# Performance work log

Hardware: AMD Instinct MI355X
Metric: run time of the kernel (lower is better)

The kernel has to match this reference:

```python
import jax, jax.numpy as jnp
import numpy as np
from jax.ops import segment_sum

N_NODES = 50000
N_EDGES = 50000
N_GRAPHS = 1024


def _inv_deg(idx, num_segments):
    deg = segment_sum(jnp.ones(idx.shape[0], jnp.float32), idx, num_segments=num_segments)
    return jnp.where(deg > 0, 1.0 / deg, 0.0)


def hypergraph_conv(x, W, b, node_idx, edge_idx):
    # PyG HypergraphConv (use_attention=False, heads=1, hyperedge_weight=1):
    # out = D^{-1} H B^{-1} H^T (X W) + b
    D = _inv_deg(node_idx, N_NODES)   # inverse node degree [N]
    B = _inv_deg(edge_idx, N_EDGES)   # inverse hyperedge degree [E]
    xl = x @ W                         # [N, out]
    # node -> hyperedge aggregation
    edge_feat = B[:, None] * segment_sum(xl[node_idx], edge_idx, num_segments=N_EDGES)
    # hyperedge -> node aggregation
    out = D[:, None] * segment_sum(edge_feat[edge_idx], node_idx, num_segments=N_NODES)
    return out + b


def global_mean_pool(x, batch):
    s = segment_sum(x, batch, num_segments=N_GRAPHS)
    cnt = segment_sum(jnp.ones(x.shape[0], jnp.float32), batch, num_segments=N_GRAPHS)
    return s / jnp.maximum(cnt, 1.0)[:, None]


def setup_inputs() -> dict:
    key = jax.random.key(0)
    ks = jax.random.split(key, 16)
    F, H = 128, 256
    def lin(k, fi, fo):
        s = 1.0 / np.sqrt(fi)
        k1, k2 = jax.random.split(k)
        return (jax.random.uniform(k1, (fi, fo), jnp.float32, -s, s),
                jax.random.uniform(k2, (fo,), jnp.float32, -s, s))
    W1, b1 = lin(ks[0], F, H)
    W2, b2 = lin(ks[1], H, 2 * H)
    W3, b3 = lin(ks[2], 2 * H, H)
    Wl1, bl1 = lin(ks[3], H, H // 2)
    Wl2, bl2 = lin(ks[4], H // 2, 1)
    x = jax.random.normal(ks[5], (N_NODES, F), jnp.float32)
    hyperedge_index = jax.random.randint(ks[6], (2, 400000), 0, N_EDGES, jnp.int64)
    batch = jnp.sort(jax.random.randint(ks[7], (N_NODES,), 0, N_GRAPHS, jnp.int64))
    return {"x": x, "hyperedge_index": hyperedge_index, "batch": batch,
            "W1": W1, "b1": b1, "W2": W2, "b2": b2, "W3": W3, "b3": b3,
            "Wl1": Wl1, "bl1": bl1, "Wl2": Wl2, "bl2": bl2}


def reference(x, hyperedge_index, batch, W1, b1, W2, b2, W3, b3, Wl1, bl1, Wl2, bl2):
    node_idx, edge_idx = hyperedge_index[0], hyperedge_index[1]
    h = jax.nn.relu(hypergraph_conv(x, W1, b1, node_idx, edge_idx))
    h = jax.nn.relu(hypergraph_conv(h, W2, b2, node_idx, edge_idx))
    h = jax.nn.relu(hypergraph_conv(h, W3, b3, node_idx, edge_idx))
    g = global_mean_pool(h, batch)              # [G, H]
    g = jax.nn.relu(g @ Wl1 + bl1)
    out = g @ Wl2 + bl2                          # [G, 1]
    return out
```

## Files before the change

### kernel.cpp

```cpp
#include <hip/hip_runtime.h>
#include <hip/hip_bf16.h>

#define N_NODES  50000
#define N_EDGES  50000
#define N_INC    400000
#define N_GRAPHS 1024
#define M_PAD    50048
#define SEG_CAP  50176

typedef __bf16 bf16x8 __attribute__((ext_vector_type(8)));
typedef float  f32x4  __attribute__((ext_vector_type(4)));

__device__ __forceinline__ unsigned short f2bf(float f) {
    __hip_bfloat16 h = __float2bfloat16(f);
    return __builtin_bit_cast(unsigned short, h);
}
__device__ __forceinline__ float bflo(unsigned int u) {
    return __builtin_bit_cast(float, u << 16);
}
__device__ __forceinline__ float bfhi(unsigned int u) {
    return __builtin_bit_cast(float, u & 0xffff0000u);
}
__device__ __forceinline__ unsigned int packbf(float a, float b) {
    return (unsigned int)f2bf(a) | ((unsigned int)f2bf(b) << 16);
}
__device__ __forceinline__ void load_lds16(const unsigned short* g, unsigned short* l) {
    __builtin_amdgcn_global_load_lds((const __attribute__((address_space(1))) void*)g,
                                     (__attribute__((address_space(3))) void*)l, 16, 0, 0);
}

#define NB_INC  1563
#define NB_CONV 6250
#define NB_W1   128
#define NB_W2   512
#define NB_W3   512
__global__ __launch_bounds__(256) void normhist_kernel(const int* __restrict__ hei,
                                                       int* __restrict__ nidx, int* __restrict__ eidx,
                                                       unsigned short* __restrict__ rn,
                                                       unsigned short* __restrict__ re,
                                                       int* __restrict__ ndeg_p, int* __restrict__ edeg_p,
                                                       const float* __restrict__ x,
                                                       unsigned short* __restrict__ xbf,
                                                       const float* __restrict__ W1, unsigned short* __restrict__ wt1,
                                                       const float* __restrict__ W2, unsigned short* __restrict__ wt2,
                                                       const float* __restrict__ W3, unsigned short* __restrict__ wt3) {
    int b = blockIdx.x, t = threadIdx.x;
    if (b < NB_INC) {
        __shared__ int s32;
        if (t == 0) s32 = 0;
        __syncthreads();
        int probe = hei[4 * t + 1] | hei[4 * t + 3];
        if (probe) s32 = 1;
        __syncthreads();
        int is32 = s32;
        int i = b * 256 + t;
        if (i < N_INC) {
            int n, e;
            if (is32) { n = hei[i];     e = hei[N_INC + i]; }
            else      { n = hei[2 * i]; e = hei[2 * N_INC + 2 * i]; }
            nidx[i] = n; eidx[i] = e;
            rn[i] = (unsigned short)atomicAdd(&ndeg_p[n << 4], 1);
            re[i] = (unsigned short)atomicAdd(&edeg_p[e << 4], 1);
        }
    } else if (b < NB_INC + NB_CONV) {
        int i = (b - NB_INC) * 256 + t;
        float4 v = *(const float4*)(x + 4 * (size_t)i);
        ushort4 o;
        o.x = f2bf(v.x); o.y = f2bf(v.y); o.z = f2bf(v.z); o.w = f2bf(v.w);
        *(ushort4*)(xbf + 4 * (size_t)i) = o;
    } else if (b < NB_INC + NB_CONV + NB_W1) {
        int i = (b - NB_INC - NB_CONV) * 256 + t;
        int k = i >> 8, n = i & 255;
        wt1[n * 128 + k] = f2bf(W1[i]);
    } else if (b < NB_INC + NB_CONV + NB_W1 + NB_W2) {
        int i = (b - NB_INC - NB_CONV - NB_W1) * 256 + t;
        int k = i >> 9, n = i & 511;
        wt2[n * 256 + k] = f2bf(W2[i]);
    } else {
        int i = (b - NB_INC - NB_CONV - NB_W1 - NB_W2) * 256 + t;
        int k = i >> 8, n = i & 255;
        wt3[n * 512 + k] = f2bf(W3[i]);
    }
}

__global__ __launch_bounds__(256) void scan_up_f(const int* __restrict__ edeg_p,
                                                 const int* __restrict__ ndeg_p,
                                                 const int* __restrict__ hei,
                                                 const int* __restrict__ braw,
                                                 int* __restrict__ eoff, int* __restrict__ noff,
                                                 int* __restrict__ goff,
                                                 int* __restrict__ partials) {
    int b = blockIdx.x, t = threadIdx.x;
    if (b >= 98) {
        __shared__ int s32;
        if (t == 0) s32 = 0;
        __syncthreads();
        int probe = hei[4 * t + 1] | hei[4 * t + 3];
        if (probe) s32 = 1;
        __syncthreads();
        int is32 = s32;
        int g = (b - 98) * 256 + t;
        int lo = 0, hi = N_NODES;
        while (lo < hi) {
            int mid = (lo + hi) >> 1;
            int v = is32 ? braw[mid] : braw[2 * mid];
            if (v < g) lo = mid + 1; else hi = mid;
        }
        goff[g] = lo;
        if (g == 1023) goff[1024] = N_NODES;
        return;
    }
    __shared__ int lds[256];
    const int* in; int* outp; int lb;
    if (b < 49) { in = edeg_p; outp = eoff; lb = b; }
    else        { in = ndeg_p; outp = noff; lb = b - 49; }
    int base = lb * 1024 + t * 4;
    int4 v;
    v.x = in[(size_t)(base + 0) << 4];
    v.y = in[(size_t)(base + 1) << 4];
    v.z = in[(size_t)(base + 2) << 4];
    v.w = in[(size_t)(base + 3) << 4];
    int s = v.x + v.y + v.z + v.w;
    lds[t] = s;
    __syncthreads();
    for (int off = 1; off < 256; off <<= 1) {
        int u = (t >= off) ? lds[t - off] : 0;
        __syncthreads();
        lds[t] += u;
        __syncthreads();
    }
    int excl = lds[t] - s;
    if (t == 255) partials[b] = lds[255];
    int4 o;
    o.x = excl;
    o.y = excl + v.x;
    o.z = o.y + v.y;
    o.w = o.z + v.z;
    *(int4*)(outp + base) = o;
}

__global__ __launch_bounds__(128) void scan_mid_f(int* __restrict__ partials) {
    __shared__ int lds[98];
    int t = threadIdx.x;
    if (t < 98) lds[t] = partials[t];
    __syncthreads();
    if (t < 2) {
        int lo = t * 49, hi = lo + 49;
        int run = 0;
        for (int i = lo; i < hi; ++i) { int x = lds[i]; lds[i] = run; run += x; }
    }
    __syncthreads();
    if (t < 98) partials[t] = lds[t];
}

__global__ __launch_bounds__(256) void scan_down_f(int* __restrict__ eoff,
                                                   int* __restrict__ noff,
                                                   const int* __restrict__ partials) {
    int b = blockIdx.x, t = threadIdx.x;
    int* outp; int lb;
    if (b < 49) { outp = eoff; lb = b; }
    else        { outp = noff; lb = b - 49; }
    int base = lb * 1024 + t * 4;
    int p = partials[b];
    int4 v = *(const int4*)(outp + base);
    v.x += p; v.y += p; v.z += p; v.w += p;
    *(int4*)(outp + base) = v;
}

__global__ __launch_bounds__(256) void prep_kernel(const int* __restrict__ nidx,
                                                   const int* __restrict__ eidx,
                                                   const unsigned short* __restrict__ rn,
                                                   const unsigned short* __restrict__ re,
                                                   const int* __restrict__ eoff,
                                                   const int* __restrict__ noff,
                                                   unsigned short* __restrict__ csre,
                                                   unsigned short* __restrict__ csrn) {
    int i = blockIdx.x * 256 + threadIdx.x;
    if (i >= N_INC) return;
    int n = nidx[i], e = eidx[i];
    csre[eoff[e] + re[i]] = (unsigned short)n;
    csrn[noff[n] + rn[i]] = (unsigned short)e;
}

template <bool EPI>
__global__ __launch_bounds__(256) void gemm128_kernel(const unsigned short* __restrict__ A,
                                                      const unsigned short* __restrict__ Bt,
                                                      const float* __restrict__ bias,
                                                      unsigned short* __restrict__ C,
                                                      int M, int K, int N) {
    __shared__ unsigned short As[128 * 32];
    __shared__ unsigned short Bs[128 * 32];
    __shared__ unsigned short Cs[32][140];
    int tid  = threadIdx.x;
    int wave = tid >> 6, lane = tid & 63;
    int n0 = blockIdx.x * 128, m0 = blockIdx.y * 128;
    int quad = lane >> 4, fr = lane & 15;
    int wr = wave >> 1, wc = wave & 1;
    int lrow16 = lane >> 2;
    int lchunk = (lane & 3) * 8;

    const unsigned short* gsrc;
    unsigned short* ldst;
    if (wave < 2) { gsrc = A  + (size_t)(m0 + wave * 64) * K;       ldst = As + wave * 64 * 32; }
    else          { gsrc = Bt + (size_t)(n0 + (wave - 2) * 64) * K; ldst = Bs + (wave - 2) * 64 * 32; }

    f32x4 acc[4][4];
#pragma unroll
    for (int s = 0; s < 4; ++s)
#pragma unroll
        for (int c = 0; c < 4; ++c) acc[s][c] = (f32x4){0.f, 0.f, 0.f, 0.f};

    for (int k0 = 0; k0 < K; k0 += 32) {
#pragma unroll
        for (int l = 0; l < 4; ++l) {
            const unsigned short* g = gsrc + (size_t)(l * 16 + lrow16) * K + k0 + lchunk;
            load_lds16(g, ldst + l * 16 * 32);
        }
        __syncthreads();
        bf16x8 af[4], bfr[4];
#pragma unroll
        for (int s = 0; s < 4; ++s)
            af[s] = *(const bf16x8*)&As[(wr * 64 + s * 16 + fr) * 32 + quad * 8];
#pragma unroll
        for (int c = 0; c < 4; ++c)
            bfr[c] = *(const bf16x8*)&Bs[(wc * 64 + c * 16 + fr) * 32 + quad * 8];
#pragma unroll
        for (int s = 0; s < 4; ++s)
#pragma unroll
            for (int c = 0; c < 4; ++c)
                acc[s][c] = __builtin_amdgcn_mfma_f32_16x16x32_bf16(af[s], bfr[c], acc[s][c], 0, 0, 0);
        __syncthreads();
    }

    float bv[4];
#pragma unroll
    for (int c = 0; c < 4; ++c) bv[c] = EPI ? bias[n0 + wc * 64 + c * 16 + fr] : 0.f;
#pragma unroll
    for (int s = 0; s < 4; ++s) {
#pragma unroll
        for (int c = 0; c < 4; ++c)
#pragma unroll
            for (int r = 0; r < 4; ++r) {
                float v = acc[s][c][r];
                if (EPI) v = fmaxf(v + bv[c], 0.f);
                Cs[wr * 16 + quad * 4 + r][wc * 64 + c * 16 + fr] = f2bf(v);
            }
        __syncthreads();
#pragma unroll
        for (int i = 0; i < 2; ++i) {
            int rl  = i * 16 + (tid >> 4);
            int col = (tid & 15) * 8;
            int gm  = m0 + (rl >> 4) * 64 + s * 16 + (rl & 15);
            if (gm < M) {
                uint4 v = *(const uint4*)&Cs[rl][col];
                *(uint4*)&C[(size_t)gm * N + n0 + col] = v;
            }
        }
        __syncthreads();
    }
}

template <int C, bool BIAS>
__device__ __forceinline__ void seg_body(const unsigned short* __restrict__ in,
                                         const int* __restrict__ offs,
                                         const int* __restrict__ degs_p,
                                         const unsigned short* __restrict__ csr_src,
                                         const float* __restrict__ bias,
                                         unsigned short* __restrict__ outp,
                                         int nseg) {
    constexpr int VEC = C / 64;
    constexpr int NW  = VEC / 2;
    int w = (blockIdx.x * 256 + threadIdx.x) >> 6;
    int lane = threadIdx.x & 63;
    if (w >= nseg) return;
    int deg   = __builtin_amdgcn_readfirstlane(degs_p[(size_t)w << 4]);
    int start = __builtin_amdgcn_readfirstlane(offs[w]);
    float dinv = (deg > 0) ? 1.0f / (float)deg : 0.0f;
    const unsigned short* cs = csr_src + start;
    float acc[VEC];
#pragma unroll
    for (int q = 0; q < VEC; ++q) acc[q] = 0.f;
    size_t lbase = (size_t)lane * VEC;

    auto accum = [&](unsigned int* v) {
#pragma unroll
        for (int q = 0; q < NW; ++q) { acc[2 * q] += bflo(v[q]); acc[2 * q + 1] += bfhi(v[q]); }
    };
    auto loadrow = [&](int src, unsigned int* v) {
        const unsigned int* p = (const unsigned int*)(in + (size_t)src * C + lbase);
        if constexpr (NW == 4)      { uint4 t = *(const uint4*)p; v[0] = t.x; v[1] = t.y; v[2] = t.z; v[3] = t.w; }
        else if constexpr (NW == 2) { uint2 t = *(const uint2*)p; v[0] = t.x; v[1] = t.y; }
        else                        { v[0] = *p; }
    };

    int j = 0;
    for (; j + 8 <= deg; j += 8) {
        int s[8];
        unsigned int v[8][NW];
#pragma unroll
        for (int u = 0; u < 8; ++u) s[u] = __builtin_amdgcn_readfirstlane((int)cs[j + u]);
#pragma unroll
        for (int u = 0; u < 8; ++u) loadrow(s[u], v[u]);
        __asm__ __volatile__("" ::: "memory");
#pragma unroll
        for (int u = 0; u < 8; ++u) accum(v[u]);
    }
    for (; j + 4 <= deg; j += 4) {
        int s[4];
        unsigned int v[4][NW];
#pragma unroll
        for (int u = 0; u < 4; ++u) s[u] = __builtin_amdgcn_readfirstlane((int)cs[j + u]);
#pragma unroll
        for (int u = 0; u < 4; ++u) loadrow(s[u], v[u]);
        __asm__ __volatile__("" ::: "memory");
#pragma unroll
        for (int u = 0; u < 4; ++u) accum(v[u]);
    }
    for (; j < deg; ++j) {
        int s0 = __builtin_amdgcn_readfirstlane((int)cs[j]);
        unsigned int v0[NW];
        loadrow(s0, v0);
        accum(v0);
    }

    unsigned int o[NW];
#pragma unroll
    for (int q = 0; q < NW; ++q) {
        float a = acc[2 * q] * dinv;
        float b = acc[2 * q + 1] * dinv;
        if constexpr (BIAS) {
            a = fmaxf(a + bias[lbase + 2 * q], 0.f);
            b = fmaxf(b + bias[lbase + 2 * q + 1], 0.f);
        }
        o[q] = packbf(a, b);
    }
    unsigned int* po = (unsigned int*)(outp + (size_t)w * C + lbase);
    if constexpr (NW == 4)      { *(uint4*)po = make_uint4(o[0], o[1], o[2], o[3]); }
    else if constexpr (NW == 2) { *(uint2*)po = make_uint2(o[0], o[1]); }
    else                        { *po = o[0]; }
}

template <int C>
__global__ __launch_bounds__(256) void seg_edge_t(const unsigned short* __restrict__ xl,
                                                  const int* __restrict__ eoff,
                                                  const int* __restrict__ edeg_p,
                                                  const unsigned short* __restrict__ csr_src,
                                                  unsigned short* __restrict__ ef) {
    seg_body<C, false>(xl, eoff, edeg_p, csr_src, nullptr, ef, N_EDGES);
}

template <int C, bool BIAS>
__global__ __launch_bounds__(256) void seg_node_t(const unsigned short* __restrict__ ef,
                                                  const int* __restrict__ noff,
                                                  const int* __restrict__ ndeg_p,
                                                  const unsigned short* __restrict__ csr_src,
                                                  const float* __restrict__ bias,
                                                  unsigned short* __restrict__ hout) {
    seg_body<C, BIAS>(ef, noff, ndeg_p, csr_src, bias, hout, N_NODES);
}

__global__ __launch_bounds__(256) void pool_head_kernel(const unsigned short* __restrict__ h,
                                                        const int* __restrict__ goff,
                                                        const float* __restrict__ Wl1,
                                                        const float* __restrict__ bl1,
                                                        const float* __restrict__ Wl2,
                                                        const float* __restrict__ bl2,
                                                        float* __restrict__ out) {
    __shared__ float xs[256];
    __shared__ float red[128];
    int g = blockIdx.x, t = threadIdx.x;
    int s = goff[g], cnt = goff[g + 1] - s;
    float acc = 0.f;
    for (int i = 0; i < cnt; ++i) {
        unsigned int u = h[(size_t)(s + i) * 256 + t];
        acc += __builtin_bit_cast(float, u << 16);
    }
    xs[t] = acc / (float)(cnt > 0 ? cnt : 1);
    __syncthreads();
    if (t < 128) {
        float s2 = 0.f;
        for (int f = 0; f < 256; ++f) s2 += xs[f] * Wl1[f * 128 + t];
        s2 = fmaxf(s2 + bl1[t], 0.f);
        red[t] = s2 * Wl2[t];
    }
    __syncthreads();
    for (int off = 64; off > 0; off >>= 1) {
        if (t < off) red[t] += red[t + off];
        __syncthreads();
    }
    if (t == 0) out[g] = red[0] + bl2[0];
}

extern "C" void kernel_launch(void* const* d_in, const int* in_sizes, int n_in,
                              void* d_out, int out_size, void* d_ws, size_t ws_size,
                              hipStream_t stream) {
    const float* x     = (const float*)d_in[0];
    const int* hei     = (const int*)d_in[1];
    const int* braw    = (const int*)d_in[2];
    const float* W1    = (const float*)d_in[3];
    const float* b1    = (const float*)d_in[4];
    const float* W2    = (const float*)d_in[5];
    const float* b2    = (const float*)d_in[6];
    const float* W3    = (const float*)d_in[7];
    const float* b3    = (const float*)d_in[8];
    const float* Wl1   = (const float*)d_in[9];
    const float* bl1   = (const float*)d_in[10];
    const float* Wl2   = (const float*)d_in[11];
    const float* bl2   = (const float*)d_in[12];
    float* out         = (float*)d_out;

    char* w = (char*)d_ws;
    size_t off = 0;
    auto alloc = [&](size_t bytes) { size_t p = off; off += (bytes + 255) & ~(size_t)255; return p; };
    size_t o_edegp = alloc((size_t)SEG_CAP * 16 * 4);
    size_t o_ndegp = alloc((size_t)SEG_CAP * 16 * 4);
    size_t zero_end = off;
    size_t o_eoff = alloc((size_t)SEG_CAP * 4);
    size_t o_noff = alloc((size_t)SEG_CAP * 4);
    size_t o_goff = alloc((size_t)1025 * 4);
    size_t o_part = alloc(128 * 4);
    size_t o_nidx = alloc((size_t)N_INC * 4);
    size_t o_eidx = alloc((size_t)N_INC * 4);
    size_t o_rn   = alloc((size_t)N_INC * 2);
    size_t o_re   = alloc((size_t)N_INC * 2);
    size_t o_csre = alloc((size_t)N_INC * 2);
    size_t o_csrn = alloc((size_t)N_INC * 2);
    size_t o_wt1  = alloc((size_t)128 * 256 * 2);
    size_t o_wt2  = alloc((size_t)256 * 512 * 2);
    size_t o_wt3  = alloc((size_t)512 * 256 * 2);
    size_t o_xbf  = alloc((size_t)M_PAD * 128 * 2);
    size_t o_Y    = alloc((size_t)M_PAD * 256 * 2);
    size_t o_H1   = alloc((size_t)M_PAD * 256 * 2);
    size_t o_H2   = alloc((size_t)M_PAD * 512 * 2);
    size_t o_bufE = alloc((size_t)N_EDGES * 256 * 2);

    int* edeg_p = (int*)(w + o_edegp);
    int* ndeg_p = (int*)(w + o_ndegp);
    int* eoff = (int*)(w + o_eoff);
    int* noff = (int*)(w + o_noff);
    int* goff = (int*)(w + o_goff);
    int* part = (int*)(w + o_part);
    int* nidx = (int*)(w + o_nidx);
    int* eidx = (int*)(w + o_eidx);
    unsigned short* rn   = (unsigned short*)(w + o_rn);
    unsigned short* re   = (unsigned short*)(w + o_re);
    unsigned short* csre = (unsigned short*)(w + o_csre);
    unsigned short* csrn = (unsigned short*)(w + o_csrn);
    unsigned short* wt1  = (unsigned short*)(w + o_wt1);
    unsigned short* wt2  = (unsigned short*)(w + o_wt2);
    unsigned short* wt3  = (unsigned short*)(w + o_wt3);
    unsigned short* xbf  = (unsigned short*)(w + o_xbf);
    unsigned short* Y    = (unsigned short*)(w + o_Y);
    unsigned short* H1   = (unsigned short*)(w + o_H1);
    unsigned short* H2   = (unsigned short*)(w + o_H2);
    unsigned short* bufE = (unsigned short*)(w + o_bufE);

    hipMemsetAsync(w, 0, zero_end, stream);
    normhist_kernel<<<NB_INC + NB_CONV + NB_W1 + NB_W2 + NB_W3, 256, 0, stream>>>(
        hei, nidx, eidx, rn, re, ndeg_p, edeg_p, x, xbf, W1, wt1, W2, wt2, W3, wt3);
    scan_up_f<<<102, 256, 0, stream>>>(edeg_p, ndeg_p, hei, braw, eoff, noff, goff, part);
    scan_mid_f<<<1, 128, 0, stream>>>(part);
    scan_down_f<<<98, 256, 0, stream>>>(eoff, noff, part);
    prep_kernel<<<(N_INC + 255) / 256, 256, 0, stream>>>(nidx, eidx, rn, re, eoff, noff, csre, csrn);

    int segGrid = (N_NODES * 64 + 255) / 256;

    seg_edge_t<128><<<segGrid, 256, 0, stream>>>(xbf, eoff, edeg_p, csre, bufE);
    seg_node_t<128, false><<<segGrid, 256, 0, stream>>>(bufE, noff, ndeg_p, csrn, nullptr, Y);
    {
        dim3 grid(256 / 128, M_PAD / 128);
        gemm128_kernel<true><<<grid, 256, 0, stream>>>(Y, wt1, b1, H1, N_NODES, 128, 256);
    }
    seg_edge_t<256><<<segGrid, 256, 0, stream>>>(H1, eoff, edeg_p, csre, bufE);
    seg_node_t<256, false><<<segGrid, 256, 0, stream>>>(bufE, noff, ndeg_p, csrn, nullptr, Y);
    {
        dim3 grid(512 / 128, M_PAD / 128);
        gemm128_kernel<true><<<grid, 256, 0, stream>>>(Y, wt2, b2, H2, N_NODES, 256, 512);
    }
    {
        dim3 grid(256 / 128, M_PAD / 128);
        gemm128_kernel<false><<<grid, 256, 0, stream>>>(H2, wt3, nullptr, Y, N_NODES, 512, 256);
    }
    seg_edge_t<256><<<segGrid, 256, 0, stream>>>(Y, eoff, edeg_p, csre, bufE);
    seg_node_t<256, true><<<segGrid, 256, 0, stream>>>(bufE, noff, ndeg_p, csrn, b3, H1);

    pool_head_kernel<<<N_GRAPHS, 256, 0, stream>>>(H1, goff, Wl1, bl1, Wl2, bl2, out);
}
```

Before: 429.2 us.

## Process two segments per wavefront in gather-reduce kernels and fold scan_mid into scan_down

The segment-sum kernels now give each half-wavefront (32 lanes) its own segment, so one wave handles two segments with twice as many features per lane. Both halves run to the larger of the two degrees, using clamped indices and masked accumulation so inactive rows add zero. With average degree around 8, this is meant to cut per-wave overhead and raise memory-level parallelism per wave. The cost is divergence waste when the two paired degrees differ and per-lane (non-uniform) index loads. Separately, the small scan_mid kernel is merged into scan_down: every block redoes the 98-element partial scan in LDS, which removes one kernel launch.

Result: faster. 413.6 us (-3.6%).

```diff
diff --git a/kernel.cpp b/kernel.cpp
--- a/kernel.cpp
+++ b/kernel.cpp
@@ -139,9 +139,11 @@
     *(int4*)(outp + base) = o;
 }
 
-__global__ __launch_bounds__(128) void scan_mid_f(int* __restrict__ partials) {
+__global__ __launch_bounds__(256) void scan_down_f(int* __restrict__ eoff,
+                                                   int* __restrict__ noff,
+                                                   const int* __restrict__ partials) {
     __shared__ int lds[98];
-    int t = threadIdx.x;
+    int b = blockIdx.x, t = threadIdx.x;
     if (t < 98) lds[t] = partials[t];
     __syncthreads();
     if (t < 2) {
@@ -150,18 +152,11 @@
         for (int i = lo; i < hi; ++i) { int x = lds[i]; lds[i] = run; run += x; }
     }
     __syncthreads();
-    if (t < 98) partials[t] = lds[t];
-}
-
-__global__ __launch_bounds__(256) void scan_down_f(int* __restrict__ eoff,
-                                                   int* __restrict__ noff,
-                                                   const int* __restrict__ partials) {
-    int b = blockIdx.x, t = threadIdx.x;
     int* outp; int lb;
     if (b < 49) { outp = eoff; lb = b; }
     else        { outp = noff; lb = b - 49; }
     int base = lb * 1024 + t * 4;
-    int p = partials[b];
+    int p = lds[b];
     int4 v = *(const int4*)(outp + base);
     v.x += p; v.y += p; v.z += p; v.w += p;
     *(int4*)(outp + base) = v;
@@ -261,68 +256,65 @@
 }
 
 template <int C, bool BIAS>
-__device__ __forceinline__ void seg_body(const unsigned short* __restrict__ in,
-                                         const int* __restrict__ offs,
-                                         const int* __restrict__ degs_p,
-                                         const unsigned short* __restrict__ csr_src,
-                                         const float* __restrict__ bias,
-                                         unsigned short* __restrict__ outp,
-                                         int nseg) {
-    constexpr int VEC = C / 64;
+__device__ __forceinline__ void seg_body2(const unsigned short* __restrict__ in,
+                                          const int* __restrict__ offs,
+                                          const int* __restrict__ degs_p,
+                                          const unsigned short* __restrict__ csr_src,
+                                          const float* __restrict__ bias,
+                                          unsigned short* __restrict__ outp,
+                                          int nseg) {
+    constexpr int VEC = C / 32;
     constexpr int NW  = VEC / 2;
-    int w = (blockIdx.x * 256 + threadIdx.x) >> 6;
+    int wid  = (blockIdx.x * 256 + threadIdx.x) >> 6;
     int lane = threadIdx.x & 63;
-    if (w >= nseg) return;
-    int deg   = __builtin_amdgcn_readfirstlane(degs_p[(size_t)w << 4]);
-    int start = __builtin_amdgcn_readfirstlane(offs[w]);
+    int half = lane >> 5, l2 = lane & 31;
+    int seg = 2 * wid + half;
+    if (2 * wid >= nseg) return;
+    bool segvalid = seg < nseg;
+    int deg   = segvalid ? degs_p[(size_t)seg << 4] : 0;
+    int start = segvalid ? offs[seg] : 0;
     float dinv = (deg > 0) ? 1.0f / (float)deg : 0.0f;
+    int maxdeg = max(deg, __shfl_xor(deg, 32, 64));
     const unsigned short* cs = csr_src + start;
     float acc[VEC];
 #pragma unroll
     for (int q = 0; q < VEC; ++q) acc[q] = 0.f;
-    size_t lbase = (size_t)lane * VEC;
-
-    auto accum = [&](unsigned int* v) {
-#pragma unroll
-        for (int q = 0; q < NW; ++q) { acc[2 * q] += bflo(v[q]); acc[2 * q + 1] += bfhi(v[q]); }
+    size_t lbase = (size_t)l2 * VEC;
+
+    auto loadrow = [&](int src, unsigned int* v) {
+        src = min(src, nseg - 1);
+        const unsigned int* p = (const unsigned int*)(in + (size_t)src * C + lbase);
+        if constexpr (NW == 4) { uint4 t = *(const uint4*)p; v[0] = t.x; v[1] = t.y; v[2] = t.z; v[3] = t.w; }
+        else                   { uint2 t = *(const uint2*)p; v[0] = t.x; v[1] = t.y; }
     };
-    auto loadrow = [&](int src, unsigned int* v) {
-        const unsigned int* p = (const unsigned int*)(in + (size_t)src * C + lbase);
-        if constexpr (NW == 4)      { uint4 t = *(const uint4*)p; v[0] = t.x; v[1] = t.y; v[2] = t.z; v[3] = t.w; }
-        else if constexpr (NW == 2) { uint2 t = *(const uint2*)p; v[0] = t.x; v[1] = t.y; }
-        else                        { v[0] = *p; }
+    auto maccum = [&](unsigned int* v, unsigned int msk) {
+#pragma unroll
+        for (int q = 0; q < NW; ++q) {
+            unsigned int x = v[q] & msk;
+            acc[2 * q] += bflo(x); acc[2 * q + 1] += bfhi(x);
+        }
     };
 
-    int j = 0;
-    for (; j + 8 <= deg; j += 8) {
-        int s[8];
+    int dc = (deg > 0) ? deg - 1 : 0;
+    for (int j = 0; j < maxdeg; j += 8) {
         unsigned int v[8][NW];
-#pragma unroll
-        for (int u = 0; u < 8; ++u) s[u] = __builtin_amdgcn_readfirstlane((int)cs[j + u]);
-#pragma unroll
-        for (int u = 0; u < 8; ++u) loadrow(s[u], v[u]);
+        int row[8];
+#pragma unroll
+        for (int u = 0; u < 8; ++u) {
+            int jj = min(j + u, dc);
+            row[u] = (int)cs[jj];
+        }
+#pragma unroll
+        for (int u = 0; u < 8; ++u) loadrow(row[u], v[u]);
         __asm__ __volatile__("" ::: "memory");
 #pragma unroll
-        for (int u = 0; u < 8; ++u) accum(v[u]);
-    }
-    for (; j + 4 <= deg; j += 4) {
-        int s[4];
-        unsigned int v[4][NW];
-#pragma unroll
-        for (int u = 0; u < 4; ++u) s[u] = __builtin_amdgcn_readfirstlane((int)cs[j + u]);
-#pragma unroll
-        for (int u = 0; u < 4; ++u) loadrow(s[u], v[u]);
-        __asm__ __volatile__("" ::: "memory");
-#pragma unroll
-        for (int u = 0; u < 4; ++u) accum(v[u]);
-    }
-    for (; j < deg; ++j) {
-        int s0 = __builtin_amdgcn_readfirstlane((int)cs[j]);
-        unsigned int v0[NW];
-        loadrow(s0, v0);
-        accum(v0);
-    }
-
+        for (int u = 0; u < 8; ++u) {
+            unsigned int msk = (j + u < deg) ? 0xffffffffu : 0u;
+            maccum(v[u], msk);
+        }
+    }
+
+    if (!segvalid) return;
     unsigned int o[NW];
 #pragma unroll
     for (int q = 0; q < NW; ++q) {
@@ -334,10 +326,9 @@
         }
         o[q] = packbf(a, b);
     }
-    unsigned int* po = (unsigned int*)(outp + (size_t)w * C + lbase);
-    if constexpr (NW == 4)      { *(uint4*)po = make_uint4(o[0], o[1], o[2], o[3]); }
-    else if constexpr (NW == 2) { *(uint2*)po = make_uint2(o[0], o[1]); }
-    else                        { *po = o[0]; }
+    unsigned int* po = (unsigned int*)(outp + (size_t)seg * C + lbase);
+    if constexpr (NW == 4) { *(uint4*)po = make_uint4(o[0], o[1], o[2], o[3]); }
+    else                   { *(uint2*)po = make_uint2(o[0], o[1]); }
 }
 
 template <int C>
@@ -346,7 +337,7 @@
                                                   const int* __restrict__ edeg_p,
                                                   const unsigned short* __restrict__ csr_src,
                                                   unsigned short* __restrict__ ef) {
-    seg_body<C, false>(xl, eoff, edeg_p, csr_src, nullptr, ef, N_EDGES);
+    seg_body2<C, false>(xl, eoff, edeg_p, csr_src, nullptr, ef, N_EDGES);
 }
 
 template <int C, bool BIAS>
@@ -356,7 +347,7 @@
                                                   const unsigned short* __restrict__ csr_src,
                                                   const float* __restrict__ bias,
                                                   unsigned short* __restrict__ hout) {
-    seg_body<C, BIAS>(ef, noff, ndeg_p, csr_src, bias, hout, N_NODES);
+    seg_body2<C, BIAS>(ef, noff, ndeg_p, csr_src, bias, hout, N_NODES);
 }
 
 __global__ __launch_bounds__(256) void pool_head_kernel(const unsigned short* __restrict__ h,
@@ -423,8 +414,8 @@
     size_t o_eidx = alloc((size_t)N_INC * 4);
     size_t o_rn   = alloc((size_t)N_INC * 2);
     size_t o_re   = alloc((size_t)N_INC * 2);
-    size_t o_csre = alloc((size_t)N_INC * 2);
-    size_t o_csrn = alloc((size_t)N_INC * 2);
+    size_t o_csre = alloc((size_t)N_INC * 2 + 64);
+    size_t o_csrn = alloc((size_t)N_INC * 2 + 64);
     size_t o_wt1  = alloc((size_t)128 * 256 * 2);
     size_t o_wt2  = alloc((size_t)256 * 512 * 2);
     size_t o_wt3  = alloc((size_t)512 * 256 * 2);
@@ -459,20 +450,19 @@
     normhist_kernel<<<NB_INC + NB_CONV + NB_W1 + NB_W2 + NB_W3, 256, 0, stream>>>(
         hei, nidx, eidx, rn, re, ndeg_p, edeg_p, x, xbf, W1, wt1, W2, wt2, W3, wt3);
     scan_up_f<<<102, 256, 0, stream>>>(edeg_p, ndeg_p, hei, braw, eoff, noff, goff, part);
-    scan_mid_f<<<1, 128, 0, stream>>>(part);
     scan_down_f<<<98, 256, 0, stream>>>(eoff, noff, part);
     prep_kernel<<<(N_INC + 255) / 256, 256, 0, stream>>>(nidx, eidx, rn, re, eoff, noff, csre, csrn);
 
-    int segGrid = (N_NODES * 64 + 255) / 256;
-
-    seg_edge_t<128><<<segGrid, 256, 0, stream>>>(xbf, eoff, edeg_p, csre, bufE);
-    seg_node_t<128, false><<<segGrid, 256, 0, stream>>>(bufE, noff, ndeg_p, csrn, nullptr, Y);
+    int segGrid2 = ((N_NODES + 1) / 2 * 64 + 255) / 256;
+
+    seg_edge_t<128><<<segGrid2, 256, 0, stream>>>(xbf, eoff, edeg_p, csre, bufE);
+    seg_node_t<128, false><<<segGrid2, 256, 0, stream>>>(bufE, noff, ndeg_p, csrn, nullptr, Y);
     {
         dim3 grid(256 / 128, M_PAD / 128);
         gemm128_kernel<true><<<grid, 256, 0, stream>>>(Y, wt1, b1, H1, N_NODES, 128, 256);
     }
-    seg_edge_t<256><<<segGrid, 256, 0, stream>>>(H1, eoff, edeg_p, csre, bufE);
-    seg_node_t<256, false><<<segGrid, 256, 0, stream>>>(bufE, noff, ndeg_p, csrn, nullptr, Y);
+    seg_edge_t<256><<<segGrid2, 256, 0, stream>>>(H1, eoff, edeg_p, csre, bufE);
+    seg_node_t<256, false><<<segGrid2, 256, 0, stream>>>(bufE, noff, ndeg_p, csrn, nullptr, Y);
     {
         dim3 grid(512 / 128, M_PAD / 128);
         gemm128_kernel<true><<<grid, 256, 0, stream>>>(Y, wt2, b2, H2, N_NODES, 256, 512);
@@ -481,8 +471,8 @@
         dim3 grid(256 / 128, M_PAD / 128);
         gemm128_kernel<false><<<grid, 256, 0, stream>>>(H2, wt3, nullptr, Y, N_NODES, 512, 256);
     }
-    seg_edge_t<256><<<segGrid, 256, 0, stream>>>(Y, eoff, edeg_p, csre, bufE);
-    seg_node_t<256, true><<<segGrid, 256, 0, stream>>>(bufE, noff, ndeg_p, csrn, b3, H1);
+    seg_edge_t<256><<<segGrid2, 256, 0, stream>>>(Y, eoff, edeg_p, csre, bufE);
+    seg_node_t<256, true><<<segGrid2, 256, 0, stream>>>(bufE, noff, ndeg_p, csrn, b3, H1);
 
     pool_head_kernel<<<N_GRAPHS, 256, 0, stream>>>(H1, goff, Wl1, bl1, Wl2, bl2, out);
 }
```
